# Kernel optimization log

Hardware: AMD Instinct MI355X
Metric: run time of the kernel (lower is better)

Reference implementation:

```python
import jax, jax.numpy as jnp
import numpy as np

D_EMB = 1024
B, T = 8, 2048

def setup_inputs() -> dict:
    key = jax.random.key(0)
    ks = jax.random.split(key, 7)
    s = 0.02
    return {
        "x": jax.random.normal(ks[0], (B, T, D_EMB), dtype=jnp.float32),
        "W_attn": jax.random.normal(ks[1], (3 * D_EMB, D_EMB), dtype=jnp.float32) * s,
        "b_attn": jax.random.normal(ks[2], (3 * D_EMB,), dtype=jnp.float32) * s,
        "W_proj": jax.random.normal(ks[3], (D_EMB, D_EMB), dtype=jnp.float32) * s,
        "b_proj": jax.random.normal(ks[4], (D_EMB,), dtype=jnp.float32) * s,
        "W_fc": jax.random.normal(ks[5], (1, D_EMB), dtype=jnp.float32) * s,
        "b_fc": jax.random.normal(ks[6], (1,), dtype=jnp.float32) * s,
    }

def reference(x, W_attn, b_attn, W_proj, b_proj, W_fc, b_fc):
    # qkv projection: torch Linear => x @ W.T + b
    qkv = jnp.einsum('btc,dc->btd', x, W_attn) + b_attn          # [B,T,3C]
    q, k, v = jnp.split(qkv, 3, axis=2)                          # each [B,T,C]
    scale = q.shape[-1] ** (-0.5)
    attn_scores = jnp.einsum('btc,bsc->bts', q, k) * scale       # [B,T,T]
    attn_weights = jax.nn.softmax(attn_scores, axis=-1)          # traditional softmax
    y = jnp.einsum('bts,bsc->btc', attn_weights, v)              # [B,T,C]
    y = jnp.einsum('btc,dc->btd', y, W_proj) + b_proj            # [B,T,C]
    out = jnp.einsum('btc,oc->bto', y, W_fc) + b_fc              # [B,T,1]
    return out
```

## Files before the change

### kernel.cpp

```cpp
#include <hip/hip_runtime.h>
#include <stdint.h>

#define D_EMB 1024
#define NBATCH 8
#define SEQ 2048
#define MTOT (NBATCH*SEQ)

typedef __attribute__((ext_vector_type(8))) short short8;
typedef __attribute__((ext_vector_type(4))) float f32x4;

__device__ __forceinline__ ushort bf16r(float x) {
  union { float f; uint32_t u; } c; c.f = x;
  return (ushort)((c.u + 0x7fffu + ((c.u >> 16) & 1u)) >> 16);
}

__device__ __forceinline__ void cp16(const ushort* g, ushort* l) {
  __builtin_amdgcn_global_load_lds(
      (const __attribute__((address_space(1))) void*)g,
      (__attribute__((address_space(3))) void*)l, 16, 0, 0);
}

__global__ __launch_bounds__(256) void cvt_w(
    const float4* __restrict__ Wattn4, const float* __restrict__ bproj,
    const float* __restrict__ Wfc, const float* __restrict__ bfc,
    ushort* __restrict__ wt, float* __restrict__ w_eff, float* __restrict__ wv_eff,
    float* __restrict__ v_eff, float4* __restrict__ numden4, float* __restrict__ sc) {
  int tid = threadIdx.x;
  int b = blockIdx.x;
  __shared__ ushort lt[64][68];
  __shared__ float red[4];
  if (b < 512) {
    int td = b & 31, tc = b >> 5;
    #pragma unroll
    for (int rep = 0; rep < 4; rep++) {
      int i = (tid >> 4) + rep * 16;
      int jj = tid & 15;
      float4 v = Wattn4[(long)(td * 64 + i) * 256 + tc * 16 + jj];
      lt[i][jj * 4 + 0] = bf16r(v.x);
      lt[i][jj * 4 + 1] = bf16r(v.y);
      lt[i][jj * 4 + 2] = bf16r(v.z);
      lt[i][jj * 4 + 3] = bf16r(v.w);
    }
    __syncthreads();
    #pragma unroll
    for (int rep = 0; rep < 2; rep++) {
      int c = (tid >> 3) + rep * 32;
      int d0 = (tid & 7) * 8;
      short8 o;
      #pragma unroll
      for (int k = 0; k < 8; k++) o[k] = (short)lt[d0 + k][c];
      *(short8*)(wt + (long)(tc * 64 + c) * 2048 + td * 64 + d0) = o;
    }
    return;
  }
  int b2 = b - 512;
  if (b2 == 0) {
    for (int i = tid; i < 1024; i += 256) { w_eff[i] = 0.f; wv_eff[i] = 0.f; v_eff[i] = 0.f; }
    return;
  }
  if (b2 == 1) {
    float v = 0.f;
    #pragma unroll
    for (int i = 0; i < 4; i++) { int c = tid + i * 256; v += bproj[c] * Wfc[c]; }
    int lane = tid & 63, w = tid >> 6;
    #pragma unroll
    for (int off = 32; off; off >>= 1) v += __shfl_xor(v, off);
    if (lane == 0) red[w] = v;
    __syncthreads();
    if (tid == 0) sc[0] = red[0] + red[1] + red[2] + red[3] + bfc[0];
    return;
  }
  numden4[(long)(b2 - 2) * 256 + tid] = make_float4(0.f, 0.f, 0.f, 0.f);
}

template<int MODE>
__device__ __forceinline__ void gemm_body(
    int bx, int by, int z, ushort* lds_a, ushort* lds_b,
    const ushort* __restrict__ A, long lda, long sAz,
    const ushort* __restrict__ B, long ldb, long sBz,
    ushort* __restrict__ C, long ldc, float* __restrict__ fC, float scale, int K,
    const float* __restrict__ vw, const float* __restrict__ bb,
    float* __restrict__ num, float* __restrict__ den) {
  const ushort* Az = A + (long)z * sAz;
  const ushort* Bz = B + (long)z * sBz;
  long m0 = (long)by * 128, n0 = (long)bx * 128;
  int t = threadIdx.x;
  int wave = t >> 6, lane = t & 63;
  int r = lane & 15, q = lane >> 4;
  int wm = (wave & 1) * 64, wn = (wave >> 1) * 64;

  f32x4 acc[4][4] = {};

  int row0 = t >> 3;
  int kc = (t & 7) ^ (row0 & 7);
  const ushort* Ap = Az + (m0 + row0) * lda + kc * 8;
  const ushort* Bp = Bz + (n0 + row0) * ldb + kc * 8;
  long a32 = 32 * lda, b32 = 32 * ldb;

  int swz = r & 7;

  #pragma unroll 1
  for (int k0 = 0; k0 < K; k0 += 64) {
    if (k0) __syncthreads();
    cp16(Ap + k0,            lds_a + t * 8);
    cp16(Ap + k0 + a32,      lds_a + (t + 256) * 8);
    cp16(Ap + k0 + 2 * a32,  lds_a + (t + 512) * 8);
    cp16(Ap + k0 + 3 * a32,  lds_a + (t + 768) * 8);
    cp16(Bp + k0,            lds_b + t * 8);
    cp16(Bp + k0 + b32,      lds_b + (t + 256) * 8);
    cp16(Bp + k0 + 2 * b32,  lds_b + (t + 512) * 8);
    cp16(Bp + k0 + 3 * b32,  lds_b + (t + 768) * 8);
    __syncthreads();
    #pragma unroll
    for (int kk = 0; kk < 2; kk++) {
      int cidx = (kk * 4 + q) ^ swz;
      short8 af[4], bf[4];
      #pragma unroll
      for (int i = 0; i < 4; i++)
        af[i] = *(const short8*)(lds_a + ((wm + i * 16 + r) * 8 + cidx) * 8);
      #pragma unroll
      for (int j = 0; j < 4; j++)
        bf[j] = *(const short8*)(lds_b + ((wn + j * 16 + r) * 8 + cidx) * 8);
      #pragma unroll
      for (int i = 0; i < 4; i++)
        #pragma unroll
        for (int j = 0; j < 4; j++)
          acc[i][j] = __builtin_amdgcn_mfma_f32_16x16x32_bf16(af[i], bf[j], acc[i][j], 0, 0, 0);
    }
  }

  if (MODE == 0) {
    #pragma unroll
    for (int i = 0; i < 4; i++) {
      #pragma unroll
      for (int j = 0; j < 4; j++) {
        long col = n0 + wn + j * 16 + r;
        #pragma unroll
        for (int rr = 0; rr < 4; rr++) {
          long row = m0 + wm + i * 16 + q * 4 + rr;
          C[row * ldc + col] = bf16r(acc[i][j][rr] * scale);
        }
      }
    }
  } else if (MODE == 2) {
    float* fz = fC + (long)z * 1048576;
    #pragma unroll
    for (int i = 0; i < 4; i++) {
      #pragma unroll
      for (int j = 0; j < 4; j++) {
        long col = n0 + wn + j * 16 + r;
        #pragma unroll
        for (int rr = 0; rr < 4; rr++) {
          long row = m0 + wm + i * 16 + q * 4 + rr;
          fz[row * 1024 + col] = acc[i][j][rr];
        }
      }
    }
  } else {
    const float* vwz = vw + (long)z * SEQ + n0;
    const float* bbz = bb + (long)z * SEQ + n0;
    float* numz = num + (long)z * SEQ + m0;
    float* denz = den + (long)z * SEQ + m0;
    float vwj[4], bbj[4];
    #pragma unroll
    for (int j = 0; j < 4; j++) {
      vwj[j] = vwz[wn + j * 16 + r];
      bbj[j] = bbz[wn + j * 16 + r];
    }
    #pragma unroll
    for (int i = 0; i < 4; i++) {
      #pragma unroll
      for (int rr = 0; rr < 4; rr++) {
        float sn = 0.f, sd = 0.f;
        #pragma unroll
        for (int j = 0; j < 4; j++) {
          float e = __expf((acc[i][j][rr] + bbj[j]) * scale);
          sd += e;
          sn += e * vwj[j];
        }
        #pragma unroll
        for (int off = 1; off < 16; off <<= 1) {
          sn += __shfl_xor(sn, off);
          sd += __shfl_xor(sd, off);
        }
        if (r == 0) {
          int row = wm + i * 16 + q * 4 + rr;
          atomicAdd(&numz[row], sn);
          atomicAdd(&denz[row], sd);
        }
      }
    }
  }
}

__global__ __launch_bounds__(256, 4) void prep1mt(
    const float* __restrict__ Wp, const float* __restrict__ Wfc,
    const float* __restrict__ Wattn, const float* __restrict__ battn,
    float* __restrict__ w_eff, float* __restrict__ v_eff,
    const ushort* __restrict__ wt, float* __restrict__ mtf) {
  __shared__ __align__(16) ushort lds_a[128 * 64];
  __shared__ __align__(16) ushort lds_b[128 * 64];
  int b = blockIdx.x;
  if (b < 512) {
    int c = (b & 3) * 256 + threadIdx.x;
    int y = b >> 2;
    if (y < 64) {
      int d0 = y * 16;
      float s = 0.f;
      #pragma unroll
      for (int d = d0; d < d0 + 16; d++) s += Wfc[d] * Wp[(long)d * D_EMB + c];
      atomicAdd(&w_eff[c], s);
    } else {
      int d0 = (y - 64) * 16;
      float s = 0.f;
      #pragma unroll
      for (int d = d0; d < d0 + 16; d++) s += battn[d] * Wattn[(long)(1024 + d) * D_EMB + c];
      atomicAdd(&v_eff[c], s);
    }
    return;
  }
  int m = b - 512;
  int kz = m >> 6, g = m & 63;
  gemm_body<2>(g & 7, g >> 3, kz, lds_a, lds_b,
               wt + 1024, 2048L, 128L, wt, 2048L, 128L,
               nullptr, 0L, mtf, 1.0f, 128, nullptr, nullptr, nullptr, nullptr);
}

__global__ __launch_bounds__(256) void prep2red(
    const float* __restrict__ Wattn, const float* __restrict__ battn,
    const float* __restrict__ w_eff, float* __restrict__ wv_eff,
    float* __restrict__ sc, const float4* __restrict__ mtf4, ushort* __restrict__ mt) {
  int tid = threadIdx.x;
  int y = blockIdx.y;
  if (y < 64) {
    int d = blockIdx.x * 256 + tid;
    int c0 = y * 16;
    float s = 0.f;
    #pragma unroll
    for (int c = c0; c < c0 + 16; c++) s += w_eff[c] * Wattn[(long)(2048 + c) * D_EMB + d];
    atomicAdd(&wv_eff[d], s);
    return;
  }
  if (y == 64) {
    if (blockIdx.x != 0) return;
    float v = 0.f;
    #pragma unroll
    for (int i = 0; i < 4; i++) { int c = tid + i * 256; v += battn[2048 + c] * w_eff[c]; }
    int lane = tid & 63, w = tid >> 6;
    #pragma unroll
    for (int off = 32; off; off >>= 1) v += __shfl_xor(v, off);
    __shared__ float red[4];
    if (lane == 0) red[w] = v;
    __syncthreads();
    if (tid == 0) sc[1] = red[0] + red[1] + red[2] + red[3];
    return;
  }
  int seg = (y - 65) * 4 + blockIdx.x;
  #pragma unroll
  for (int jj = 0; jj < 4; jj++) {
    long p4 = (long)seg * 1024 + tid + 256 * jj;
    float4 s = mtf4[p4];
    #pragma unroll
    for (int kz = 1; kz < 8; kz++) {
      float4 t2 = mtf4[(long)kz * 262144 + p4];
      s.x += t2.x; s.y += t2.y; s.z += t2.z; s.w += t2.w;
    }
    *(ushort4*)(mt + p4 * 4) = make_ushort4(bf16r(s.x), bf16r(s.y), bf16r(s.z), bf16r(s.w));
  }
}

__global__ __launch_bounds__(256) void cvt_x(
    const float4* __restrict__ x4, const float4* __restrict__ wv4,
    const float4* __restrict__ v4, const float* __restrict__ sc,
    ushort* __restrict__ xb, float* __restrict__ vw, float* __restrict__ bb) {
  int tid = threadIdx.x;
  int wave = tid >> 6, lane = tid & 63;
  long row = (long)blockIdx.x * 4 + wave;
  const float4* xr = x4 + row * 256;
  ushort* xo = xb + row * D_EMB;
  float s = 0.f, s2 = 0.f;
  #pragma unroll
  for (int i = 0; i < 4; i++) {
    int idx = lane + i * 64;
    float4 v = xr[idx];
    float4 w = wv4[idx];
    float4 u = v4[idx];
    *(ushort4*)(xo + idx * 4) = make_ushort4(bf16r(v.x), bf16r(v.y), bf16r(v.z), bf16r(v.w));
    s  += v.x * w.x + v.y * w.y + v.z * w.z + v.w * w.w;
    s2 += v.x * u.x + v.y * u.y + v.z * u.z + v.w * u.w;
  }
  #pragma unroll
  for (int off = 32; off; off >>= 1) { s += __shfl_xor(s, off); s2 += __shfl_xor(s2, off); }
  if (lane == 0) { vw[row] = s + sc[1]; bb[row] = s2; }
}

template<int MODE, int RMODE>
__global__ __launch_bounds__(256, 4) void gemm_nt(
    const ushort* __restrict__ A, long lda, long sAz,
    const ushort* __restrict__ B, long ldb, long sBz,
    ushort* __restrict__ C, long ldc, float scale, int K,
    const float* __restrict__ vw, const float* __restrict__ bb,
    float* __restrict__ num, float* __restrict__ den) {
  __shared__ __align__(16) ushort lds_a[128 * 64];
  __shared__ __align__(16) ushort lds_b[128 * 64];
  int bx, by, z;
  if (RMODE == 1) {
    int f = (int)(blockIdx.x + 8u * blockIdx.y);
    int xcd = f & 7, g = f >> 3;
    by = xcd * 16 + (g & 15); bx = g >> 4; z = 0;
  } else {
    bx = blockIdx.x; by = blockIdx.y; z = blockIdx.z;
  }
  gemm_body<MODE>(bx, by, z, lds_a, lds_b, A, lda, sAz, B, ldb, sBz,
                  C, ldc, nullptr, scale, K, vw, bb, num, den);
}

__global__ __launch_bounds__(256) void finalize(
    const float* __restrict__ num, const float* __restrict__ den,
    const float* __restrict__ sc, float* __restrict__ out) {
  long i = blockIdx.x * 256L + threadIdx.x;
  out[i] = num[i] / den[i] + sc[0];
}

extern "C" void kernel_launch(void* const* d_in, const int* in_sizes, int n_in,
                              void* d_out, int out_size, void* d_ws, size_t ws_size,
                              hipStream_t stream) {
  const float* x     = (const float*)d_in[0];
  const float* Wattn = (const float*)d_in[1];
  const float* battn = (const float*)d_in[2];
  const float* Wproj = (const float*)d_in[3];
  const float* bproj = (const float*)d_in[4];
  const float* Wfc   = (const float*)d_in[5];
  const float* bfc   = (const float*)d_in[6];
  float* out = (float*)d_out;

  const size_t OFF_XB    = 0;
  const size_t OFF_WT    = 33554432;
  const size_t OFF_MT    = 37748736;
  const size_t OFF_XM    = 39845888;
  const size_t OFF_MTF   = OFF_XM;
  const size_t OFF_NUM   = 73400320;
  const size_t OFF_DEN   = 73465856;
  const size_t OFF_VW    = 73531392;
  const size_t OFF_BB    = 73596928;
  const size_t OFF_WEFF  = 73662464;
  const size_t OFF_WVEFF = 73666560;
  const size_t OFF_VEFF  = 73670656;
  const size_t OFF_SC    = 73674752;
  const size_t NEED      = 73674760;
  if (ws_size < NEED) return;

  char* ws = (char*)d_ws;
  ushort* xb    = (ushort*)(ws + OFF_XB);
  ushort* wt    = (ushort*)(ws + OFF_WT);
  ushort* mt    = (ushort*)(ws + OFF_MT);
  ushort* xm    = (ushort*)(ws + OFF_XM);
  float* mtf    = (float*)(ws + OFF_MTF);
  float* num    = (float*)(ws + OFF_NUM);
  float* den    = (float*)(ws + OFF_DEN);
  float* vw     = (float*)(ws + OFF_VW);
  float* bb     = (float*)(ws + OFF_BB);
  float* w_eff  = (float*)(ws + OFF_WEFF);
  float* wv_eff = (float*)(ws + OFF_WVEFF);
  float* v_eff  = (float*)(ws + OFF_VEFF);
  float* sc     = (float*)(ws + OFF_SC);

  cvt_w<<<dim3(546), dim3(256), 0, stream>>>(
      (const float4*)Wattn, bproj, Wfc, bfc, wt, w_eff, wv_eff, v_eff, (float4*)num, sc);

  prep1mt<<<dim3(1024), dim3(256), 0, stream>>>(
      Wproj, Wfc, Wattn, battn, w_eff, v_eff, wt, mtf);

  prep2red<<<dim3(4, 129), dim3(256), 0, stream>>>(
      Wattn, battn, w_eff, wv_eff, sc, (const float4*)mtf, mt);

  cvt_x<<<dim3(4096), dim3(256), 0, stream>>>(
      (const float4*)x, (const float4*)wv_eff, (const float4*)v_eff, sc, xb, vw, bb);

  gemm_nt<0, 1><<<dim3(8, 128, 1), dim3(256), 0, stream>>>(
      xb, (long)D_EMB, 0L, mt, (long)D_EMB, 0L,
      xm, (long)D_EMB, 1.0f, D_EMB, nullptr, nullptr, nullptr, nullptr);

  gemm_nt<1, 0><<<dim3(16, 16, NBATCH), dim3(256), 0, stream>>>(
      xm, (long)D_EMB, (long)SEQ * D_EMB, xb, (long)D_EMB, (long)SEQ * D_EMB,
      nullptr, 0L, 0.03125f, D_EMB, vw, bb, num, den);

  finalize<<<dim3(64), dim3(256), 0, stream>>>(num, den, sc, out);
}
```

Before: 264.2 us.

## Merge prep kernels into three stages with partial-sum buffers instead of atomics

Restructures the weight-preprocessing chain from four launches into three. The w_eff and v_eff vector-matrix products now write per-chunk partials to new buffers instead of using atomics. Those partials are reduced inside the next stage alongside the Wq^T Wk GEMM, and the mtf reduction is folded into the x conversion kernel. This removes one launch and one dependency barrier, but adds extra partial-buffer traffic and redundant re-reduction of pw in several blocks.

```diff
diff --git a/kernel.cpp b/kernel.cpp
--- a/kernel.cpp
+++ b/kernel.cpp
@@ -18,59 +18,6 @@
   __builtin_amdgcn_global_load_lds(
       (const __attribute__((address_space(1))) void*)g,
       (__attribute__((address_space(3))) void*)l, 16, 0, 0);
-}
-
-__global__ __launch_bounds__(256) void cvt_w(
-    const float4* __restrict__ Wattn4, const float* __restrict__ bproj,
-    const float* __restrict__ Wfc, const float* __restrict__ bfc,
-    ushort* __restrict__ wt, float* __restrict__ w_eff, float* __restrict__ wv_eff,
-    float* __restrict__ v_eff, float4* __restrict__ numden4, float* __restrict__ sc) {
-  int tid = threadIdx.x;
-  int b = blockIdx.x;
-  __shared__ ushort lt[64][68];
-  __shared__ float red[4];
-  if (b < 512) {
-    int td = b & 31, tc = b >> 5;
-    #pragma unroll
-    for (int rep = 0; rep < 4; rep++) {
-      int i = (tid >> 4) + rep * 16;
-      int jj = tid & 15;
-      float4 v = Wattn4[(long)(td * 64 + i) * 256 + tc * 16 + jj];
-      lt[i][jj * 4 + 0] = bf16r(v.x);
-      lt[i][jj * 4 + 1] = bf16r(v.y);
-      lt[i][jj * 4 + 2] = bf16r(v.z);
-      lt[i][jj * 4 + 3] = bf16r(v.w);
-    }
-    __syncthreads();
-    #pragma unroll
-    for (int rep = 0; rep < 2; rep++) {
-      int c = (tid >> 3) + rep * 32;
-      int d0 = (tid & 7) * 8;
-      short8 o;
-      #pragma unroll
-      for (int k = 0; k < 8; k++) o[k] = (short)lt[d0 + k][c];
-      *(short8*)(wt + (long)(tc * 64 + c) * 2048 + td * 64 + d0) = o;
-    }
-    return;
-  }
-  int b2 = b - 512;
-  if (b2 == 0) {
-    for (int i = tid; i < 1024; i += 256) { w_eff[i] = 0.f; wv_eff[i] = 0.f; v_eff[i] = 0.f; }
-    return;
-  }
-  if (b2 == 1) {
-    float v = 0.f;
-    #pragma unroll
-    for (int i = 0; i < 4; i++) { int c = tid + i * 256; v += bproj[c] * Wfc[c]; }
-    int lane = tid & 63, w = tid >> 6;
-    #pragma unroll
-    for (int off = 32; off; off >>= 1) v += __shfl_xor(v, off);
-    if (lane == 0) red[w] = v;
-    __syncthreads();
-    if (tid == 0) sc[0] = red[0] + red[1] + red[2] + red[3] + bfc[0];
-    return;
-  }
-  numden4[(long)(b2 - 2) * 256 + tid] = make_float4(0.f, 0.f, 0.f, 0.f);
 }
 
 template<int MODE>
@@ -193,89 +140,164 @@
   }
 }
 
-__global__ __launch_bounds__(256, 4) void prep1mt(
+__global__ __launch_bounds__(256) void d1_init(
+    const float4* __restrict__ Wattn4,
     const float* __restrict__ Wp, const float* __restrict__ Wfc,
     const float* __restrict__ Wattn, const float* __restrict__ battn,
-    float* __restrict__ w_eff, float* __restrict__ v_eff,
+    const float* __restrict__ bproj, const float* __restrict__ bfc,
+    ushort* __restrict__ wt, float* __restrict__ pw, float* __restrict__ pv,
+    float* __restrict__ wv_eff, float4* __restrict__ numden4, float* __restrict__ sc) {
+  int tid = threadIdx.x;
+  int b = blockIdx.x;
+  __shared__ ushort lt[64][68];
+  __shared__ float red[4];
+  if (b < 512) {
+    int td = b & 31, tc = b >> 5;
+    #pragma unroll
+    for (int rep = 0; rep < 4; rep++) {
+      int i = (tid >> 4) + rep * 16;
+      int jj = tid & 15;
+      float4 v = Wattn4[(long)(td * 64 + i) * 256 + tc * 16 + jj];
+      lt[i][jj * 4 + 0] = bf16r(v.x);
+      lt[i][jj * 4 + 1] = bf16r(v.y);
+      lt[i][jj * 4 + 2] = bf16r(v.z);
+      lt[i][jj * 4 + 3] = bf16r(v.w);
+    }
+    __syncthreads();
+    #pragma unroll
+    for (int rep = 0; rep < 2; rep++) {
+      int c = (tid >> 3) + rep * 32;
+      int d0 = (tid & 7) * 8;
+      short8 o;
+      #pragma unroll
+      for (int k = 0; k < 8; k++) o[k] = (short)lt[d0 + k][c];
+      *(short8*)(wt + (long)(tc * 64 + c) * 2048 + td * 64 + d0) = o;
+    }
+    return;
+  }
+  if (b < 1024) {
+    int m = b - 512;
+    int c = (m & 3) * 256 + tid;
+    int y = m >> 2;
+    if (y < 64) {
+      int d0 = y * 16;
+      float s = 0.f;
+      #pragma unroll
+      for (int d = d0; d < d0 + 16; d++) s += Wfc[d] * Wp[(long)d * D_EMB + c];
+      pw[(long)y * 1024 + c] = s;
+    } else {
+      int y2 = y - 64;
+      int d0 = y2 * 16;
+      float s = 0.f;
+      #pragma unroll
+      for (int d = d0; d < d0 + 16; d++) s += battn[d] * Wattn[(long)(1024 + d) * D_EMB + c];
+      pv[(long)y2 * 1024 + c] = s;
+    }
+    return;
+  }
+  int b2 = b - 1024;
+  if (b2 == 0) {
+    for (int i = tid; i < 1024; i += 256) wv_eff[i] = 0.f;
+    return;
+  }
+  if (b2 == 1) {
+    float v = 0.f;
+    #pragma unroll
+    for (int i = 0; i < 4; i++) { int c = tid + i * 256; v += bproj[c] * Wfc[c]; }
+    int lane = tid & 63, w = tid >> 6;
+    #pragma unroll
+    for (int off = 32; off; off >>= 1) v += __shfl_xor(v, off);
+    if (lane == 0) red[w] = v;
+    __syncthreads();
+    if (tid == 0) sc[0] = red[0] + red[1] + red[2] + red[3] + bfc[0];
+    return;
+  }
+  numden4[(long)(b2 - 2) * 256 + tid] = make_float4(0.f, 0.f, 0.f, 0.f);
+}
+
+__global__ __launch_bounds__(256, 4) void d2_mt(
+    const float* __restrict__ Wattn, const float* __restrict__ battn,
+    const float* __restrict__ pw, const float* __restrict__ pv,
+    float* __restrict__ wv_eff, float* __restrict__ v_eff, float* __restrict__ sc,
     const ushort* __restrict__ wt, float* __restrict__ mtf) {
   __shared__ __align__(16) ushort lds_a[128 * 64];
   __shared__ __align__(16) ushort lds_b[128 * 64];
+  __shared__ float redf[16];
+  int tid = threadIdx.x;
   int b = blockIdx.x;
   if (b < 512) {
-    int c = (b & 3) * 256 + threadIdx.x;
-    int y = b >> 2;
-    if (y < 64) {
-      int d0 = y * 16;
+    int kz = b >> 6, g = b & 63;
+    gemm_body<2>(g & 7, g >> 3, kz, lds_a, lds_b,
+                 wt + 1024, 2048L, 128L, wt, 2048L, 128L,
+                 nullptr, 0L, mtf, 1.0f, 128, nullptr, nullptr, nullptr, nullptr);
+    return;
+  }
+  if (b < 768) {
+    int m = b - 512;
+    int bx = m & 3, y = m >> 2;
+    int c0 = y * 16;
+    if (tid < 16) {
       float s = 0.f;
       #pragma unroll
-      for (int d = d0; d < d0 + 16; d++) s += Wfc[d] * Wp[(long)d * D_EMB + c];
-      atomicAdd(&w_eff[c], s);
-    } else {
-      int d0 = (y - 64) * 16;
-      float s = 0.f;
-      #pragma unroll
-      for (int d = d0; d < d0 + 16; d++) s += battn[d] * Wattn[(long)(1024 + d) * D_EMB + c];
-      atomicAdd(&v_eff[c], s);
-    }
-    return;
-  }
-  int m = b - 512;
-  int kz = m >> 6, g = m & 63;
-  gemm_body<2>(g & 7, g >> 3, kz, lds_a, lds_b,
-               wt + 1024, 2048L, 128L, wt, 2048L, 128L,
-               nullptr, 0L, mtf, 1.0f, 128, nullptr, nullptr, nullptr, nullptr);
-}
-
-__global__ __launch_bounds__(256) void prep2red(
-    const float* __restrict__ Wattn, const float* __restrict__ battn,
-    const float* __restrict__ w_eff, float* __restrict__ wv_eff,
-    float* __restrict__ sc, const float4* __restrict__ mtf4, ushort* __restrict__ mt) {
-  int tid = threadIdx.x;
-  int y = blockIdx.y;
-  if (y < 64) {
-    int d = blockIdx.x * 256 + tid;
-    int c0 = y * 16;
+      for (int yp = 0; yp < 64; yp++) s += pw[(long)yp * 1024 + c0 + tid];
+      redf[tid] = s;
+    }
+    __syncthreads();
+    int d = bx * 256 + tid;
     float s = 0.f;
     #pragma unroll
-    for (int c = c0; c < c0 + 16; c++) s += w_eff[c] * Wattn[(long)(2048 + c) * D_EMB + d];
+    for (int i = 0; i < 16; i++) s += redf[i] * Wattn[(long)(2048 + c0 + i) * D_EMB + d];
     atomicAdd(&wv_eff[d], s);
     return;
   }
-  if (y == 64) {
-    if (blockIdx.x != 0) return;
+  if (b == 768) {
     float v = 0.f;
     #pragma unroll
-    for (int i = 0; i < 4; i++) { int c = tid + i * 256; v += battn[2048 + c] * w_eff[c]; }
+    for (int i = 0; i < 4; i++) {
+      int c = tid + i * 256;
+      float wc = 0.f;
+      #pragma unroll
+      for (int yp = 0; yp < 64; yp++) wc += pw[(long)yp * 1024 + c];
+      v += battn[2048 + c] * wc;
+    }
     int lane = tid & 63, w = tid >> 6;
     #pragma unroll
     for (int off = 32; off; off >>= 1) v += __shfl_xor(v, off);
-    __shared__ float red[4];
-    if (lane == 0) red[w] = v;
+    if (lane == 0) redf[w] = v;
     __syncthreads();
-    if (tid == 0) sc[1] = red[0] + red[1] + red[2] + red[3];
-    return;
-  }
-  int seg = (y - 65) * 4 + blockIdx.x;
+    if (tid == 0) sc[1] = redf[0] + redf[1] + redf[2] + redf[3];
+    return;
+  }
+  int c = (b - 769) * 256 + tid;
+  float s = 0.f;
   #pragma unroll
-  for (int jj = 0; jj < 4; jj++) {
-    long p4 = (long)seg * 1024 + tid + 256 * jj;
-    float4 s = mtf4[p4];
-    #pragma unroll
-    for (int kz = 1; kz < 8; kz++) {
-      float4 t2 = mtf4[(long)kz * 262144 + p4];
-      s.x += t2.x; s.y += t2.y; s.z += t2.z; s.w += t2.w;
-    }
-    *(ushort4*)(mt + p4 * 4) = make_ushort4(bf16r(s.x), bf16r(s.y), bf16r(s.z), bf16r(s.w));
-  }
-}
-
-__global__ __launch_bounds__(256) void cvt_x(
+  for (int yp = 0; yp < 64; yp++) s += pv[(long)yp * 1024 + c];
+  v_eff[c] = s;
+}
+
+__global__ __launch_bounds__(256) void d3_cvt(
+    const float4* __restrict__ mtf4, ushort* __restrict__ mt,
     const float4* __restrict__ x4, const float4* __restrict__ wv4,
     const float4* __restrict__ v4, const float* __restrict__ sc,
     ushort* __restrict__ xb, float* __restrict__ vw, float* __restrict__ bb) {
   int tid = threadIdx.x;
+  int b = blockIdx.x;
+  if (b < 256) {
+    #pragma unroll
+    for (int jj = 0; jj < 4; jj++) {
+      long p4 = (long)b * 1024 + tid + 256 * jj;
+      float4 s = mtf4[p4];
+      #pragma unroll
+      for (int kz = 1; kz < 8; kz++) {
+        float4 t2 = mtf4[(long)kz * 262144 + p4];
+        s.x += t2.x; s.y += t2.y; s.z += t2.z; s.w += t2.w;
+      }
+      *(ushort4*)(mt + p4 * 4) = make_ushort4(bf16r(s.x), bf16r(s.y), bf16r(s.z), bf16r(s.w));
+    }
+    return;
+  }
   int wave = tid >> 6, lane = tid & 63;
-  long row = (long)blockIdx.x * 4 + wave;
+  long row = (long)(b - 256) * 4 + wave;
   const float4* xr = x4 + row * 256;
   ushort* xo = xb + row * D_EMB;
   float s = 0.f, s2 = 0.f;
@@ -343,11 +365,12 @@
   const size_t OFF_DEN   = 73465856;
   const size_t OFF_VW    = 73531392;
   const size_t OFF_BB    = 73596928;
-  const size_t OFF_WEFF  = 73662464;
-  const size_t OFF_WVEFF = 73666560;
-  const size_t OFF_VEFF  = 73670656;
-  const size_t OFF_SC    = 73674752;
-  const size_t NEED      = 73674760;
+  const size_t OFF_PW    = 73662464;
+  const size_t OFF_PV    = 73924608;
+  const size_t OFF_WVEFF = 74186752;
+  const size_t OFF_VEFF  = 74190848;
+  const size_t OFF_SC    = 74194944;
+  const size_t NEED      = 74194952;
   if (ws_size < NEED) return;
 
   char* ws = (char*)d_ws;
@@ -360,22 +383,22 @@
   float* den    = (float*)(ws + OFF_DEN);
   float* vw     = (float*)(ws + OFF_VW);
   float* bb     = (float*)(ws + OFF_BB);
-  float* w_eff  = (float*)(ws + OFF_WEFF);
+  float* pw     = (float*)(ws + OFF_PW);
+  float* pv     = (float*)(ws + OFF_PV);
   float* wv_eff = (float*)(ws + OFF_WVEFF);
   float* v_eff  = (float*)(ws + OFF_VEFF);
   float* sc     = (float*)(ws + OFF_SC);
 
-  cvt_w<<<dim3(546), dim3(256), 0, stream>>>(
-      (const float4*)Wattn, bproj, Wfc, bfc, wt, w_eff, wv_eff, v_eff, (float4*)num, sc);
-
-  prep1mt<<<dim3(1024), dim3(256), 0, stream>>>(
-      Wproj, Wfc, Wattn, battn, w_eff, v_eff, wt, mtf);
-
-  prep2red<<<dim3(4, 129), dim3(256), 0, stream>>>(
-      Wattn, battn, w_eff, wv_eff, sc, (const float4*)mtf, mt);
-
-  cvt_x<<<dim3(4096), dim3(256), 0, stream>>>(
-      (const float4*)x, (const float4*)wv_eff, (const float4*)v_eff, sc, xb, vw, bb);
+  d1_init<<<dim3(1058), dim3(256), 0, stream>>>(
+      (const float4*)Wattn, Wproj, Wfc, Wattn, battn, bproj, bfc,
+      wt, pw, pv, wv_eff, (float4*)num, sc);
+
+  d2_mt<<<dim3(773), dim3(256), 0, stream>>>(
+      Wattn, battn, pw, pv, wv_eff, v_eff, sc, wt, mtf);
+
+  d3_cvt<<<dim3(256 + 4096), dim3(256), 0, stream>>>(
+      (const float4*)mtf, mt, (const float4*)x, (const float4*)wv_eff,
+      (const float4*)v_eff, sc, xb, vw, bb);
 
   gemm_nt<0, 1><<<dim3(8, 128, 1), dim3(256), 0, stream>>>(
       xb, (long)D_EMB, 0L, mt, (long)D_EMB, 0L,
```

Result: slower. 316.4 us (+19.8%).
